# Optimization experiments

Measured on AMD Instinct MI355X. Metric: run time of the kernel, lower is better.

The kernel has to match this reference:

```python
import jax, jax.numpy as jnp
import numpy as np

B, C, H, W = 4, 512, 32, 32
HEADS = 8
EPS = 1e-5


def setup_inputs() -> dict:
    key = jax.random.key(0)
    ks = jax.random.split(key, 9)
    s = 1.0 / np.sqrt(C)
    return {
        "x": jax.random.normal(ks[0], (B, C, H, W), dtype=jnp.float32),
        "w_q": jax.random.normal(ks[1], (C, C), dtype=jnp.float32) * s,  # Conv2d 1x1, no bias
        "w_k": jax.random.normal(ks[2], (C, C), dtype=jnp.float32) * s,
        "w_v": jax.random.normal(ks[3], (C, C), dtype=jnp.float32) * s,
        "w_head": jax.random.normal(ks[4], (HEADS, HEADS), dtype=jnp.float32) * (1.0 / np.sqrt(HEADS)),
        "in_gamma": jnp.ones((HEADS,), dtype=jnp.float32) + 0.1 * jax.random.normal(ks[5], (HEADS,), dtype=jnp.float32),
        "in_beta": 0.1 * jax.random.normal(ks[6], (HEADS,), dtype=jnp.float32),
        "w_proj": jax.random.normal(ks[7], (C, C), dtype=jnp.float32) * s,
        "b_proj": 0.02 * jax.random.normal(ks[8], (C,), dtype=jnp.float32),
    }


def reference(x, w_q, w_k, w_v, w_head, in_gamma, in_beta, w_proj, b_proj):
    b, c, h, w = x.shape
    heads = w_head.shape[0]
    hd = c // heads
    t = h * w
    scale = hd ** (-0.5)

    xf = x.reshape(b, c, t)  # [B,C,T]
    # 1x1 convs == channel matmuls
    q = jnp.einsum('oc,bct->bot', w_q, xf).reshape(b, heads, hd, t)
    k = jnp.einsum('oc,bct->bot', w_k, xf).reshape(b, heads, hd, t)
    v = jnp.einsum('oc,bct->bot', w_v, xf).reshape(b, heads, hd, t)

    attn = jnp.einsum('bhdq,bhdT->bhqT', q, k) * scale           # [B,heads,T,T]
    attn = jnp.einsum('gh,bhqT->bgqT', w_head, attn)             # head-mixing 1x1 conv
    attn = jax.nn.softmax(attn, axis=-1)
    # InstanceNorm2d over the (T,T) spatial dims, per head, biased variance
    mean = jnp.mean(attn, axis=(-2, -1), keepdims=True)
    var = jnp.var(attn, axis=(-2, -1), keepdims=True)
    attn = (attn - mean) / jnp.sqrt(var + EPS)
    attn = attn * in_gamma[None, :, None, None] + in_beta[None, :, None, None]

    out = jnp.einsum('bhqT,bhdT->bhqd', attn, v)                 # [B,heads,T,hd]
    out = out.reshape(b, t, c)                                   # same row-major flatten as torch .view
    out = out @ w_proj.T + b_proj                                # Linear
    return out.transpose(0, 2, 1).reshape(b, c, h, w)
```

## Files before the change

### kernel.cpp

```cpp
#include <hip/hip_runtime.h>
#include <hip/hip_bf16.h>

#define B_ 4
#define C_ 512
#define T_ 1024
#define SCALE_ 0.125f
#define EPS_ 1e-5f

typedef unsigned short u16;
typedef __attribute__((ext_vector_type(8))) unsigned short u16x8;
typedef __attribute__((ext_vector_type(4))) unsigned short u16x4;
typedef __attribute__((ext_vector_type(8))) short s16x8;
typedef __attribute__((ext_vector_type(4))) float f32x4;

#define QT_OFF    (0x0ull)
#define KS_OFF    (0x400000ull)
#define VS_OFF    (0x800000ull)
#define XT_OFF    (0xC00000ull)
#define O_OFF     (0x1000000ull)
#define AB_OFF    (0x1410000ull)
#define VSUM_OFF  (0x1420000ull)
#define BIAS2_OFF (0x1430000ull)
#define LSUM_OFF  (0x1440000ull)
#define L2SUM_OFF (0x1460000ull)
#define WB_OFF    (0x1480000ull)
#define LP_OFF    (0x1680000ull)
#define L2P_OFF   (0x1700000ull)
#define WS_OFF    (0x1780000ull)
#define OP_OFF    (0x2000000ull)

static __device__ __forceinline__ u16 f2bf(float f) {
  unsigned u = __float_as_uint(f);
  unsigned r = (u + 0x7fff + ((u >> 16) & 1)) >> 16;
  return (u16)r;
}
static __device__ __forceinline__ float b2f(u16 x) {
  return __uint_as_float(((unsigned)x) << 16);
}
static __device__ __forceinline__ f32x4 mfma16(s16x8 a, s16x8 b, f32x4 c) {
  return __builtin_amdgcn_mfma_f32_16x16x32_bf16(a, b, c, 0, 0, 0);
}

__global__ __launch_bounds__(256) void prep_k(
    const float* __restrict__ x, const float* __restrict__ wq,
    const float* __restrict__ wk, const float* __restrict__ wv,
    const float* __restrict__ wp, u16* __restrict__ wb,
    float* __restrict__ ws, float* __restrict__ vsum, u16* __restrict__ xt) {
  const int id = blockIdx.x;
  const int tid = threadIdx.x;
  __shared__ float Ts[64][65];
  if (id < 512) {
    const int i = (id << 8) + tid;
    const int idx = i << 3;
    const int which = idx >> 18;
    const int off = idx & 262143;
    const float* s = which == 0 ? wq : which == 1 ? wk : which == 2 ? wv : wp;
    const float4 f0 = *(const float4*)(s + off);
    const float4 f1 = *(const float4*)(s + off + 4);
    u16x8 o;
    o[0] = f2bf(f0.x); o[1] = f2bf(f0.y); o[2] = f2bf(f0.z); o[3] = f2bf(f0.w);
    o[4] = f2bf(f1.x); o[5] = f2bf(f1.y); o[6] = f2bf(f1.z); o[7] = f2bf(f1.w);
    *(u16x8*)(wb + idx) = o;
  } else if (id < 640) {
    const int idx = ((id - 512) << 8) + tid;
    if (id - 512 < 8) vsum[idx] = 0.f;
    const int o = idx >> 6, d = idx & 63;
    float s = 0.f;
#pragma unroll
    for (int j = 0; j < 8; ++j) s += wp[(o << 9) + (j << 6) + d];
    ws[idx] = s;
  } else {
    const int id3 = id - 640;
    const int b = id3 >> 7, rem = id3 & 127;
    const int t0 = (rem & 15) << 6;
    const int c0 = (rem >> 4) << 6;
    const float* __restrict__ X = x + (size_t)b * (C_ * (size_t)T_);
    u16* __restrict__ Xt = xt + (size_t)b * (T_ * (size_t)C_);
#pragma unroll
    for (int i = 0; i < 4; ++i) {
      const int e = tid + (i << 8);
      const int r = e >> 4, c4 = e & 15;
      const float4 v =
          *(const float4*)(X + (size_t)(c0 + r) * T_ + t0 + (c4 << 2));
      Ts[r][(c4 << 2) + 0] = v.x; Ts[r][(c4 << 2) + 1] = v.y;
      Ts[r][(c4 << 2) + 2] = v.z; Ts[r][(c4 << 2) + 3] = v.w;
    }
    __syncthreads();
#pragma unroll
    for (int i = 0; i < 2; ++i) {
      const int e = tid + (i << 8);
      const int tt = e >> 3, c8 = e & 7;
      u16x8 o;
#pragma unroll
      for (int j = 0; j < 8; ++j) o[j] = f2bf(Ts[(c8 << 3) + j][tt]);
      *(u16x8*)(Xt + (size_t)(t0 + tt) * C_ + c0 + (c8 << 3)) = o;
    }
  }
}

__global__ __launch_bounds__(256) void gemm_qkv(
    const u16* __restrict__ xt, const u16* __restrict__ wqb,
    const u16* __restrict__ wkb, const u16* __restrict__ wvb,
    u16* __restrict__ qto, u16* __restrict__ ks, u16* __restrict__ vs,
    float* __restrict__ vsum) {
  const int z = blockIdx.z;
  const int tid = threadIdx.x;
  const int w = tid >> 6, lane = tid & 63, lr = lane & 15, lq = lane >> 4;
  const int wm = (w >> 1) << 6, wn = (w & 1) << 5;
  __shared__ __align__(16) u16 As[128][72];
  __shared__ __align__(16) u16 Bs[64][72];
  u16* Ts = &As[0][0];
  const u16 *Ag, *Bg;
  int m0, n0, mode, b;
  if (z < 8) {
    const int which = z >> 2;
    b = z & 3;
    Ag = xt + (size_t)b * (T_ * (size_t)C_);
    m0 = blockIdx.x << 7;
    Bg = which ? wkb : wqb;
    n0 = blockIdx.y << 6;
    mode = which;
  } else {
    b = z - 8;
    const int ti = (blockIdx.y << 3) | blockIdx.x;
    Ag = wvb;
    m0 = (ti >> 4) << 7;
    Bg = xt + (size_t)b * (T_ * (size_t)C_);
    n0 = (ti & 15) << 6;
    mode = 2;
  }
  f32x4 acc[4][2] = {};
  for (int k0 = 0; k0 < C_; k0 += 64) {
#pragma unroll
    for (int it = 0; it < 4; ++it) {
      const int e = tid + (it << 8);
      const int r = e >> 3, c8 = (e & 7) << 3;
      *(u16x8*)&As[r][c8] =
          *(const u16x8*)(Ag + (size_t)(m0 + r) * C_ + k0 + c8);
    }
#pragma unroll
    for (int it = 0; it < 2; ++it) {
      const int e = tid + (it << 8);
      const int r = e >> 3, c8 = (e & 7) << 3;
      *(u16x8*)&Bs[r][c8] =
          *(const u16x8*)(Bg + (size_t)(n0 + r) * C_ + k0 + c8);
    }
    __syncthreads();
#pragma unroll
    for (int kf = 0; kf < 2; ++kf) {
      const int ko = (kf << 5) + (lq << 3);
      s16x8 a[4], bb[2];
#pragma unroll
      for (int i = 0; i < 4; ++i) a[i] = *(const s16x8*)&As[wm + (i << 4) + lr][ko];
#pragma unroll
      for (int j = 0; j < 2; ++j) bb[j] = *(const s16x8*)&Bs[wn + (j << 4) + lr][ko];
#pragma unroll
      for (int i = 0; i < 4; ++i)
#pragma unroll
        for (int j = 0; j < 2; ++j) acc[i][j] = mfma16(a[i], bb[j], acc[i][j]);
    }
    __syncthreads();
  }
  if (mode == 0) {
    u16* Y = qto + (size_t)b * (T_ * (size_t)C_);
#pragma unroll
    for (int i = 0; i < 4; ++i) {
      const int row = wm + (i << 4) + (lq << 2);
#pragma unroll
      for (int j = 0; j < 2; ++j) {
        const int col = wn + (j << 4) + lr;
#pragma unroll
        for (int r = 0; r < 4; ++r)
          Y[(size_t)(m0 + row + r) * C_ + n0 + col] =
              f2bf(acc[i][j][r] * SCALE_);
      }
    }
    return;
  }
  if (mode == 2) {
#pragma unroll
    for (int i = 0; i < 4; ++i)
#pragma unroll
      for (int r = 0; r < 4; ++r) {
        float s = acc[i][0][r] + acc[i][1][r];
        s += __shfl_xor(s, 1, 64);
        s += __shfl_xor(s, 2, 64);
        s += __shfl_xor(s, 4, 64);
        s += __shfl_xor(s, 8, 64);
        if (lr == 0) {
          const int o = m0 + wm + (i << 4) + (lq << 2) + r;
          atomicAdd(&vsum[(((b << 3) | (o >> 6)) << 6) | (o & 63)], s);
        }
      }
  }
#pragma unroll
  for (int i = 0; i < 4; ++i)
#pragma unroll
    for (int j = 0; j < 2; ++j)
#pragma unroll
      for (int r = 0; r < 4; ++r)
        Ts[(wm + (i << 4) + (lq << 2) + r) * 72 + wn + (j << 4) + lr] =
            f2bf(acc[i][j][r]);
  __syncthreads();
  const int ch = tid >> 4, part = tid & 15;
  if (mode == 1) {
    const int t32l = ch >> 2, half = (ch >> 1) & 1, fl = ch & 1;
    const int t32g = (m0 >> 5) + t32l, fg = (n0 >> 5) + fl;
    u16* dst =
        ks + (((((size_t)((b << 5) | t32g) << 1) | half) << 4 | fg) << 9);
#pragma unroll
    for (int u = 0; u < 4; ++u) {
      const int lanek = (u << 4) + part;
      const int quadk = lanek >> 4, lrk = lanek & 15;
      const int rr = ((lrk >> 2) << 3) | (half << 2) | (lrk & 3);
      const u16x8 v =
          *(const u16x8*)&Ts[((t32l << 5) + rr) * 72 + (fl << 5) + (quadk << 3)];
      *(u16x8*)(dst + (lanek << 3)) = v;
    }
  } else {
    const int gl = ch >> 3, t32l = (ch >> 2) & 1, dj = ch & 3;
    const int gg = (m0 >> 6) + gl, t32g = (n0 >> 5) + t32l;
    u16* dst =
        vs + (((((size_t)((b << 3) | gg) << 5) | t32g) << 2 | dj) << 9);
#pragma unroll
    for (int u = 0; u < 4; ++u) {
      const int lanev = (u << 4) + part;
      const int quadv = lanev >> 4, lrv = lanev & 15;
      const u16x8 v = *(const u16x8*)&Ts[((gl << 6) + (dj << 4) + lrv) * 72 +
                                         (t32l << 5) + (quadv << 3)];
      *(u16x8*)(dst + (lanev << 3)) = v;
    }
  }
}

__global__ __launch_bounds__(512, 4) void attn_fused(
    const u16* __restrict__ Qt, const u16* __restrict__ KS,
    const u16* __restrict__ VS, const float* __restrict__ wh,
    float* __restrict__ Opart, float* __restrict__ lpart,
    float* __restrict__ l2part) {
  const int id = blockIdx.x;
  const int xcd = id & 7;
  const int b = xcd >> 1;
  const int hi = id >> 3;
  const int qb = ((xcd & 1) << 5) | (hi & 31);
  const int tq = hi >> 5;
  const int q0 = qb << 4;
  const int tid = threadIdx.x;
  const int w = tid >> 6, lane = tid & 63;
  const int lr = lane & 15, quad = lane >> 4;

  __shared__ __align__(16) u16 Qs[16][522];
  __shared__ __align__(16) u16 Plds[8][16][136];
  float* Sbuf = (float*)&Plds[0][0][0];

  {
    const u16* Qb = Qt + ((size_t)b * T_ + q0) * C_;
    for (int i = tid; i < 1024; i += 512) {
      const int r = i >> 6, c8 = i & 63;
      *(u16x8*)&Qs[r][c8 << 3] = *(const u16x8*)(Qb + (size_t)r * C_ + (c8 << 3));
    }
  }

  const u16* __restrict__ Qrow = &Qs[lr][quad << 3];
  const int g = w;
  const int win = w >> 1, half = w & 1;
  const u16* __restrict__ Vc =
      VS + (((size_t)((b << 3) | g)) << 16) + (lane << 3);

  float lacc[8] = {}, l2acc[8] = {};
  f32x4 acc[4] = {};

  __syncthreads();

  for (int c = 0; c < 2; ++c) {
    const int t32k = (tq << 3) + (c << 2) + win;
    const u16* __restrict__ Kc =
        KS + (((size_t)((((b << 5) | t32k) << 1) | half)) << 13) + (lane << 3);
    f32x4 m[8] = {};
#pragma unroll 4
    for (int h = 0; h < 8; ++h) {
      f32x4 a0 = {0.f, 0.f, 0.f, 0.f};
      const s16x8 qf0 = *(const s16x8*)(Qrow + (h << 6));
      const s16x8 k0 = *(const s16x8*)(Kc + (h << 10));
      a0 = mfma16(k0, qf0, a0);
      const s16x8 qf1 = *(const s16x8*)(Qrow + (h << 6) + 32);
      const s16x8 k1 = *(const s16x8*)(Kc + (h << 10) + 512);
      a0 = mfma16(k1, qf1, a0);
#pragma unroll
      for (int gg = 0; gg < 8; ++gg) {
        const float wgh = wh[(gg << 3) + h];
        m[gg] += a0 * wgh;
      }
    }
#pragma unroll
    for (int gg = 0; gg < 8; ++gg) {
      f32x4 e0;
#pragma unroll
      for (int k = 0; k < 4; ++k) e0[k] = __expf(m[gg][k]);
      u16x4 o;
#pragma unroll
      for (int k = 0; k < 4; ++k) o[k] = f2bf(e0[k]);
      *(u16x4*)&Plds[gg][lr][(win << 5) + (quad << 3) + (half << 2)] = o;
      lacc[gg] += e0[0] + e0[1] + e0[2] + e0[3];
      l2acc[gg] += e0[0] * e0[0] + e0[1] * e0[1] + e0[2] * e0[2] + e0[3] * e0[3];
    }
    __syncthreads();
#pragma unroll
    for (int tw = 0; tw < 4; ++tw) {
      const int t32v = (tq << 3) + (c << 2) + tw;
      const s16x8 pa = *(const s16x8*)&Plds[g][lr][(tw << 5) + (quad << 3)];
#pragma unroll
      for (int dj = 0; dj < 4; ++dj) {
        const s16x8 vb =
            *(const s16x8*)(Vc + ((size_t)t32v << 11) + (dj << 9));
        acc[dj] = mfma16(pa, vb, acc[dj]);
      }
    }
    __syncthreads();
  }

  const int bg = (b << 3) + g;
  const size_t obase = ((((size_t)(tq << 5) + bg) << 10) + q0) * 64;
#pragma unroll
  for (int dj = 0; dj < 4; ++dj) {
    const int d = (dj << 4) + lr;
#pragma unroll
    for (int r = 0; r < 4; ++r) {
      const int q = (quad << 2) + r;
      Opart[obase + (size_t)q * 64 + d] = acc[dj][r];
    }
  }

  float* lbuf = Sbuf;
  float* l2buf = Sbuf + 1024;
#pragma unroll
  for (int gg = 0; gg < 8; ++gg) {
    float l = lacc[gg];
    l += __shfl_xor(l, 16, 64);
    l += __shfl_xor(l, 32, 64);
    float l2 = l2acc[gg];
    l2 += __shfl_xor(l2, 16, 64);
    l2 += __shfl_xor(l2, 32, 64);
    if (quad == 0) {
      lbuf[(w << 7) + (gg << 4) + lr] = l;
      l2buf[(w << 7) + (gg << 4) + lr] = l2;
    }
  }
  __syncthreads();
  if (lane < 16) {
    float l = 0.f, l2 = 0.f;
#pragma unroll
    for (int w2 = 0; w2 < 8; ++w2) {
      l += lbuf[(w2 << 7) + (g << 4) + lr];
      l2 += l2buf[(w2 << 7) + (g << 4) + lr];
    }
    const size_t li = (((size_t)(tq << 5) + bg) << 10) + q0 + lr;
    lpart[li] = l;
    l2part[li] = l2;
  }
}

__global__ __launch_bounds__(256) void combine_o(
    const float* __restrict__ Opart, const float* __restrict__ lpart,
    const float* __restrict__ l2part, u16* __restrict__ O,
    float* __restrict__ lsum, float* __restrict__ l2sum) {
  const int bg = blockIdx.x;
  const int qo = blockIdx.y;
  const int tid = threadIdx.x;
  const int q = (qo << 7) + (tid >> 1);
  const int d0 = (tid & 1) << 5;
  float l = 0.f, l2 = 0.f;
#pragma unroll
  for (int tq = 0; tq < 4; ++tq) {
    const size_t li = (((size_t)(tq << 5) + bg) << 10) + q;
    l += lpart[li];
    l2 += l2part[li];
  }
  const float linv = 1.f / l;
  if ((tid & 1) == 0) {
    lsum[((size_t)bg << 10) + q] = l;
    l2sum[((size_t)bg << 10) + q] = l2;
  }
  f32x4 a[8] = {};
#pragma unroll
  for (int tq = 0; tq < 4; ++tq) {
    const float* src =
        Opart + ((((size_t)(tq << 5) + bg) << 10) + q) * 64 + d0;
#pragma unroll
    for (int j = 0; j < 8; ++j) a[j] += *(const f32x4*)(src + (j << 2));
  }
  u16* dst = O + (((size_t)bg << 10) + q) * 64 + d0;
#pragma unroll
  for (int j = 0; j < 4; ++j) {
    u16x8 o;
#pragma unroll
    for (int k = 0; k < 4; ++k) {
      o[k] = f2bf(a[2 * j][k] * linv);
      o[k + 4] = f2bf(a[2 * j + 1][k] * linv);
    }
    *(u16x8*)(dst + (j << 3)) = o;
  }
}

__global__ __launch_bounds__(256) void stats_k(const float* __restrict__ lsum,
                                               const float* __restrict__ l2sum,
                                               const float* __restrict__ gamma,
                                               const float* __restrict__ beta,
                                               const float* __restrict__ ws,
                                               const float* __restrict__ bp,
                                               const float* __restrict__ vsum,
                                               float* __restrict__ ab,
                                               float* __restrict__ bias2) {
  const int bg = blockIdx.x;
  const int g = bg & 7;
  const int tid = threadIdx.x;
  const f32x4 l = *(const f32x4*)(lsum + ((size_t)bg << 10) + (tid << 2));
  const f32x4 l2 = *(const f32x4*)(l2sum + ((size_t)bg << 10) + (tid << 2));
  float ssq = 0.f;
#pragma unroll
  for (int k = 0; k < 4; ++k) ssq += l2[k] / (l[k] * l[k]);
#pragma unroll
  for (int off = 32; off; off >>= 1) ssq += __shfl_xor(ssq, off, 64);
  __shared__ float red[4];
  __shared__ float bt2s;
  if ((tid & 63) == 0) red[tid >> 6] = ssq;
  __syncthreads();
  if (tid == 0) {
    const float s = red[0] + red[1] + red[2] + red[3];
    const float mean = 0.0009765625f;
    const float var = s * (1.f / 1048576.f) - mean * mean;
    const float al = gamma[g] * rsqrtf(var + EPS_);
    const float bt2 = beta[g] - al * mean;
    ab[bg * 2] = al;
    ab[bg * 2 + 1] = bt2;
    bt2s = bt2;
  }
  __syncthreads();
  const float bt2 = bt2s;
  const float* vs = vsum + (bg << 6);
#pragma unroll
  for (int oo = 0; oo < 2; ++oo) {
    const int o = tid + (oo << 8);
    const float* wr = ws + (o << 6);
    float acc = 0.f;
#pragma unroll
    for (int d = 0; d < 64; d += 4) {
      const float4 vv4 = *(const float4*)(vs + d);
      const float4 ws4 = *(const float4*)(wr + d);
      acc += ws4.x * vv4.x + ws4.y * vv4.y + ws4.z * vv4.z + ws4.w * vv4.w;
    }
    bias2[(bg << 9) + o] = bp[o] + bt2 * acc;
  }
}

__global__ __launch_bounds__(256) void gemm_proj(const u16* __restrict__ O,
                                                 const u16* __restrict__ wpb,
                                                 const float* __restrict__ ab,
                                                 const float* __restrict__ bias2,
                                                 float* __restrict__ y) {
  const int b = blockIdx.z;
  const int m0 = blockIdx.y << 6;
  const int n0 = blockIdx.x << 6;
  const int gidx = blockIdx.x >> 1;
  const u16* __restrict__ Ob = O + (size_t)b * (8 * T_ * 64);
  __shared__ u16 As[64][72];
  __shared__ u16 Bs[64][72];
  const int tid = threadIdx.x;
  const int w = tid >> 6, lane = tid & 63, lr = lane & 15, lq = lane >> 4;
  const int mw = (w >> 1) << 5, nw = (w & 1) << 5;
  f32x4 acc[2][2] = {};
  for (int k0 = 0; k0 < C_; k0 += 64) {
#pragma unroll
    for (int it = 0; it < 2; ++it) {
      const int e = tid + (it << 8);
      const int r = e >> 3, c8 = e & 7;
      *(u16x8*)&As[r][c8 << 3] =
          *(const u16x8*)(wpb + (size_t)(m0 + r) * C_ + k0 + (c8 << 3));
      const int t = n0 + r;
      const int c = k0 + (c8 << 3);
      *(u16x8*)&Bs[r][c8 << 3] =
          *(const u16x8*)(Ob + (size_t)(t >> 7) * (T_ * 64) +
                          (size_t)(((t & 127) << 3) + (c >> 6)) * 64 + (c & 63));
    }
    __syncthreads();
#pragma unroll
    for (int kf = 0; kf < 2; ++kf) {
      const int ko = (kf << 5) + (lq << 3);
      s16x8 a[2], bb[2];
#pragma unroll
      for (int i = 0; i < 2; ++i) a[i] = *(const s16x8*)&As[mw + (i << 4) + lr][ko];
#pragma unroll
      for (int j = 0; j < 2; ++j) bb[j] = *(const s16x8*)&Bs[nw + (j << 4) + lr][ko];
#pragma unroll
      for (int i = 0; i < 2; ++i)
#pragma unroll
        for (int j = 0; j < 2; ++j) acc[i][j] = mfma16(a[i], bb[j], acc[i][j]);
    }
    __syncthreads();
  }
  const float al = ab[(((b << 3) + gidx) << 1)];
  const float* __restrict__ b2 = bias2 + (((b << 3) + gidx) << 9);
#pragma unroll
  for (int i = 0; i < 2; ++i) {
    const int row = mw + (i << 4) + (lq << 2);
#pragma unroll
    for (int j = 0; j < 2; ++j) {
      const int col = nw + (j << 4) + lr;
#pragma unroll
      for (int r = 0; r < 4; ++r)
        y[(size_t)b * (C_ * (size_t)T_) + (size_t)(m0 + row + r) * T_ + n0 + col] =
            acc[i][j][r] * al + b2[m0 + row + r];
    }
  }
}

extern "C" void kernel_launch(void* const* d_in, const int* in_sizes, int n_in,
                              void* d_out, int out_size, void* d_ws,
                              size_t ws_size, hipStream_t stream) {
  const float* x = (const float*)d_in[0];
  const float* wq = (const float*)d_in[1];
  const float* wk = (const float*)d_in[2];
  const float* wv = (const float*)d_in[3];
  const float* wh = (const float*)d_in[4];
  const float* gm = (const float*)d_in[5];
  const float* bt = (const float*)d_in[6];
  const float* wp = (const float*)d_in[7];
  const float* bp = (const float*)d_in[8];
  float* y = (float*)d_out;
  char* wsb = (char*)d_ws;

  u16* Qt = (u16*)(wsb + QT_OFF);
  u16* KS = (u16*)(wsb + KS_OFF);
  u16* VS = (u16*)(wsb + VS_OFF);
  u16* Xt = (u16*)(wsb + XT_OFF);
  u16* Og = (u16*)(wsb + O_OFF);
  float* ab = (float*)(wsb + AB_OFF);
  float* vsum = (float*)(wsb + VSUM_OFF);
  float* bias2 = (float*)(wsb + BIAS2_OFF);
  float* lsum = (float*)(wsb + LSUM_OFF);
  float* l2sum = (float*)(wsb + L2SUM_OFF);
  u16* Wb = (u16*)(wsb + WB_OFF);
  u16* WQb = Wb;
  u16* WKb = Wb + 262144;
  u16* WVb = Wb + 524288;
  u16* WPb = Wb + 786432;
  float* lpart = (float*)(wsb + LP_OFF);
  float* l2part = (float*)(wsb + L2P_OFF);
  float* ws = (float*)(wsb + WS_OFF);
  float* Opart = (float*)(wsb + OP_OFF);

  prep_k<<<dim3(1152), 256, 0, stream>>>(x, wq, wk, wv, wp, Wb, ws, vsum, Xt);
  gemm_qkv<<<dim3(8, 8, 12), 256, 0, stream>>>(Xt, WQb, WKb, WVb, Qt, KS, VS,
                                               vsum);
  attn_fused<<<dim3(1024), 512, 0, stream>>>(Qt, KS, VS, wh, Opart, lpart,
                                             l2part);
  combine_o<<<dim3(32, 8), 256, 0, stream>>>(Opart, lpart, l2part, Og, lsum,
                                             l2sum);
  stats_k<<<dim3(32), 256, 0, stream>>>(lsum, l2sum, gm, bt, ws, bp, vsum, ab,
                                        bias2);
  gemm_proj<<<dim3(16, 8, 4), 256, 0, stream>>>(Og, WPb, ab, bias2, y);
}
```

Measured before the change: 163.7 us.

## Halve attention key splits, swizzle P LDS layout, fuse stats into projection GEMM

Each attention block now processes twice as many key chunks (4 instead of 2), so the grid halves to 512 blocks and combine_o reduces only 2 partials instead of 4. The P tile stores in shared memory use an XOR swizzle on the column group to reduce bank conflicts. The separate stats kernel is removed, and each projection GEMM block recomputes the instance-norm scale, shift and bias vector for its group in a prologue. This removes one launch and the partial-sum traffic, at the cost of less attention parallelism and redundant stats work repeated in every projection block.

```diff
diff --git a/kernel.cpp b/kernel.cpp
--- a/kernel.cpp
+++ b/kernel.cpp
@@ -18,15 +18,13 @@
 #define VS_OFF    (0x800000ull)
 #define XT_OFF    (0xC00000ull)
 #define O_OFF     (0x1000000ull)
-#define AB_OFF    (0x1410000ull)
-#define VSUM_OFF  (0x1420000ull)
-#define BIAS2_OFF (0x1430000ull)
 #define LSUM_OFF  (0x1440000ull)
 #define L2SUM_OFF (0x1460000ull)
 #define WB_OFF    (0x1480000ull)
 #define LP_OFF    (0x1680000ull)
 #define L2P_OFF   (0x1700000ull)
 #define WS_OFF    (0x1780000ull)
+#define VSUM_OFF  (0x17A0000ull)
 #define OP_OFF    (0x2000000ull)
 
 static __device__ __forceinline__ u16 f2bf(float f) {
@@ -264,6 +262,7 @@
   const u16* __restrict__ Qrow = &Qs[lr][quad << 3];
   const int g = w;
   const int win = w >> 1, half = w & 1;
+  const int swz = lr & 7;
   const u16* __restrict__ Vc =
       VS + (((size_t)((b << 3) | g)) << 16) + (lane << 3);
 
@@ -272,8 +271,8 @@
 
   __syncthreads();
 
-  for (int c = 0; c < 2; ++c) {
-    const int t32k = (tq << 3) + (c << 2) + win;
+  for (int c = 0; c < 4; ++c) {
+    const int t32k = (tq << 4) + (c << 2) + win;
     const u16* __restrict__ Kc =
         KS + (((size_t)((((b << 5) | t32k) << 1) | half)) << 13) + (lane << 3);
     f32x4 m[8] = {};
@@ -292,6 +291,7 @@
         m[gg] += a0 * wgh;
       }
     }
+    const int wgrp = ((win << 2) | quad) ^ swz;
 #pragma unroll
     for (int gg = 0; gg < 8; ++gg) {
       f32x4 e0;
@@ -300,15 +300,16 @@
       u16x4 o;
 #pragma unroll
       for (int k = 0; k < 4; ++k) o[k] = f2bf(e0[k]);
-      *(u16x4*)&Plds[gg][lr][(win << 5) + (quad << 3) + (half << 2)] = o;
+      *(u16x4*)&Plds[gg][lr][(wgrp << 3) + (half << 2)] = o;
       lacc[gg] += e0[0] + e0[1] + e0[2] + e0[3];
       l2acc[gg] += e0[0] * e0[0] + e0[1] * e0[1] + e0[2] * e0[2] + e0[3] * e0[3];
     }
     __syncthreads();
 #pragma unroll
     for (int tw = 0; tw < 4; ++tw) {
-      const int t32v = (tq << 3) + (c << 2) + tw;
-      const s16x8 pa = *(const s16x8*)&Plds[g][lr][(tw << 5) + (quad << 3)];
+      const int t32v = (tq << 4) + (c << 2) + tw;
+      const int rgrp = ((tw << 2) | quad) ^ swz;
+      const s16x8 pa = *(const s16x8*)&Plds[g][lr][rgrp << 3];
 #pragma unroll
       for (int dj = 0; dj < 4; ++dj) {
         const s16x8 vb =
@@ -371,7 +372,7 @@
   const int d0 = (tid & 1) << 5;
   float l = 0.f, l2 = 0.f;
 #pragma unroll
-  for (int tq = 0; tq < 4; ++tq) {
+  for (int tq = 0; tq < 2; ++tq) {
     const size_t li = (((size_t)(tq << 5) + bg) << 10) + q;
     l += lpart[li];
     l2 += l2part[li];
@@ -383,7 +384,7 @@
   }
   f32x4 a[8] = {};
 #pragma unroll
-  for (int tq = 0; tq < 4; ++tq) {
+  for (int tq = 0; tq < 2; ++tq) {
     const float* src =
         Opart + ((((size_t)(tq << 5) + bg) << 10) + q) * 64 + d0;
 #pragma unroll
@@ -402,74 +403,62 @@
   }
 }
 
-__global__ __launch_bounds__(256) void stats_k(const float* __restrict__ lsum,
-                                               const float* __restrict__ l2sum,
-                                               const float* __restrict__ gamma,
-                                               const float* __restrict__ beta,
-                                               const float* __restrict__ ws,
-                                               const float* __restrict__ bp,
-                                               const float* __restrict__ vsum,
-                                               float* __restrict__ ab,
-                                               float* __restrict__ bias2) {
-  const int bg = blockIdx.x;
-  const int g = bg & 7;
+__global__ __launch_bounds__(256) void gemm_proj(
+    const u16* __restrict__ O, const u16* __restrict__ wpb,
+    const float* __restrict__ lsum, const float* __restrict__ l2sum,
+    const float* __restrict__ gamma, const float* __restrict__ beta,
+    const float* __restrict__ ws, const float* __restrict__ bp,
+    const float* __restrict__ vsum, float* __restrict__ y) {
+  const int b = blockIdx.z;
+  const int m0 = blockIdx.y << 6;
+  const int n0 = blockIdx.x << 6;
+  const int gidx = blockIdx.x >> 1;
+  const int bg = (b << 3) + gidx;
+  const u16* __restrict__ Ob = O + (size_t)b * (8 * T_ * 64);
+  __shared__ u16 As[64][72];
+  __shared__ u16 Bs[64][72];
+  __shared__ float red[4];
+  __shared__ float albc[2];
+  __shared__ float b2s[64];
   const int tid = threadIdx.x;
-  const f32x4 l = *(const f32x4*)(lsum + ((size_t)bg << 10) + (tid << 2));
-  const f32x4 l2 = *(const f32x4*)(l2sum + ((size_t)bg << 10) + (tid << 2));
-  float ssq = 0.f;
-#pragma unroll
-  for (int k = 0; k < 4; ++k) ssq += l2[k] / (l[k] * l[k]);
-#pragma unroll
-  for (int off = 32; off; off >>= 1) ssq += __shfl_xor(ssq, off, 64);
-  __shared__ float red[4];
-  __shared__ float bt2s;
-  if ((tid & 63) == 0) red[tid >> 6] = ssq;
+  const int w = tid >> 6, lane = tid & 63, lr = lane & 15, lq = lane >> 4;
+  const int mw = (w >> 1) << 5, nw = (w & 1) << 5;
+  {
+    const f32x4 l = *(const f32x4*)(lsum + ((size_t)bg << 10) + (tid << 2));
+    const f32x4 l2 = *(const f32x4*)(l2sum + ((size_t)bg << 10) + (tid << 2));
+    float ssq = 0.f;
+#pragma unroll
+    for (int k = 0; k < 4; ++k) ssq += l2[k] / (l[k] * l[k]);
+#pragma unroll
+    for (int off = 32; off; off >>= 1) ssq += __shfl_xor(ssq, off, 64);
+    if (lane == 0) red[w] = ssq;
+  }
   __syncthreads();
   if (tid == 0) {
     const float s = red[0] + red[1] + red[2] + red[3];
     const float mean = 0.0009765625f;
     const float var = s * (1.f / 1048576.f) - mean * mean;
-    const float al = gamma[g] * rsqrtf(var + EPS_);
-    const float bt2 = beta[g] - al * mean;
-    ab[bg * 2] = al;
-    ab[bg * 2 + 1] = bt2;
-    bt2s = bt2;
+    const float al = gamma[gidx] * rsqrtf(var + EPS_);
+    albc[0] = al;
+    albc[1] = beta[gidx] - al * mean;
   }
   __syncthreads();
-  const float bt2 = bt2s;
-  const float* vs = vsum + (bg << 6);
-#pragma unroll
-  for (int oo = 0; oo < 2; ++oo) {
-    const int o = tid + (oo << 8);
+  if (tid < 64) {
+    const int o = m0 + tid;
     const float* wr = ws + (o << 6);
+    const float* vsr = vsum + (bg << 6);
     float acc = 0.f;
 #pragma unroll
     for (int d = 0; d < 64; d += 4) {
-      const float4 vv4 = *(const float4*)(vs + d);
+      const float4 vv4 = *(const float4*)(vsr + d);
       const float4 ws4 = *(const float4*)(wr + d);
       acc += ws4.x * vv4.x + ws4.y * vv4.y + ws4.z * vv4.z + ws4.w * vv4.w;
     }
-    bias2[(bg << 9) + o] = bp[o] + bt2 * acc;
-  }
-}
-
-__global__ __launch_bounds__(256) void gemm_proj(const u16* __restrict__ O,
-                                                 const u16* __restrict__ wpb,
-                                                 const float* __restrict__ ab,
-                                                 const float* __restrict__ bias2,
-                                                 float* __restrict__ y) {
-  const int b = blockIdx.z;
-  const int m0 = blockIdx.y << 6;
-  const int n0 = blockIdx.x << 6;
-  const int gidx = blockIdx.x >> 1;
-  const u16* __restrict__ Ob = O + (size_t)b * (8 * T_ * 64);
-  __shared__ u16 As[64][72];
-  __shared__ u16 Bs[64][72];
-  const int tid = threadIdx.x;
-  const int w = tid >> 6, lane = tid & 63, lr = lane & 15, lq = lane >> 4;
-  const int mw = (w >> 1) << 5, nw = (w & 1) << 5;
+    b2s[tid] = bp[o] + albc[1] * acc;
+  }
   f32x4 acc[2][2] = {};
   for (int k0 = 0; k0 < C_; k0 += 64) {
+    if (k0 == 0) __syncthreads();
 #pragma unroll
     for (int it = 0; it < 2; ++it) {
       const int e = tid + (it << 8);
@@ -498,8 +487,7 @@
     }
     __syncthreads();
   }
-  const float al = ab[(((b << 3) + gidx) << 1)];
-  const float* __restrict__ b2 = bias2 + (((b << 3) + gidx) << 9);
+  const float al = albc[0];
 #pragma unroll
   for (int i = 0; i < 2; ++i) {
     const int row = mw + (i << 4) + (lq << 2);
@@ -509,7 +497,7 @@
 #pragma unroll
       for (int r = 0; r < 4; ++r)
         y[(size_t)b * (C_ * (size_t)T_) + (size_t)(m0 + row + r) * T_ + n0 + col] =
-            acc[i][j][r] * al + b2[m0 + row + r];
+            acc[i][j][r] * al + b2s[row + r];
     }
   }
 }
@@ -534,9 +522,7 @@
   u16* VS = (u16*)(wsb + VS_OFF);
   u16* Xt = (u16*)(wsb + XT_OFF);
   u16* Og = (u16*)(wsb + O_OFF);
-  float* ab = (float*)(wsb + AB_OFF);
   float* vsum = (float*)(wsb + VSUM_OFF);
-  float* bias2 = (float*)(wsb + BIAS2_OFF);
   float* lsum = (float*)(wsb + LSUM_OFF);
   float* l2sum = (float*)(wsb + L2SUM_OFF);
   u16* Wb = (u16*)(wsb + WB_OFF);
@@ -552,11 +538,10 @@
   prep_k<<<dim3(1152), 256, 0, stream>>>(x, wq, wk, wv, wp, Wb, ws, vsum, Xt);
   gemm_qkv<<<dim3(8, 8, 12), 256, 0, stream>>>(Xt, WQb, WKb, WVb, Qt, KS, VS,
                                                vsum);
-  attn_fused<<<dim3(1024), 512, 0, stream>>>(Qt, KS, VS, wh, Opart, lpart,
-                                             l2part);
+  attn_fused<<<dim3(512), 512, 0, stream>>>(Qt, KS, VS, wh, Opart, lpart,
+                                            l2part);
   combine_o<<<dim3(32, 8), 256, 0, stream>>>(Opart, lpart, l2part, Og, lsum,
                                              l2sum);
-  stats_k<<<dim3(32), 256, 0, stream>>>(lsum, l2sum, gm, bt, ws, bp, vsum, ab,
-                                        bias2);
-  gemm_proj<<<dim3(16, 8, 4), 256, 0, stream>>>(Og, WPb, ab, bias2, y);
-}
+  gemm_proj<<<dim3(16, 8, 4), 256, 0, stream>>>(Og, WPb, lsum, l2sum, gm, bt,
+                                                ws, bp, vsum, y);
+}
```

Result: faster. 158.6 us (-3.1%).
